# Optimization experiments

Measured on AMD Instinct MI355X. Metric: run time of the kernel, lower is better.

The kernel has to match this reference:

```python
import jax, jax.numpy as jnp
import numpy as np

N_HOPS = 2
TOPK = 10
LAMBDA = 0.5  # lambda_coeff
N_ENT = 8192
N_USR = 16384
CHANNEL = 64
N_EDGE = 1000000
NNZ = 500000
N_REL = 9


def _l2norm(x, eps=1e-12):
    # F.normalize: x / max(||x||, eps) per row
    n = jnp.linalg.norm(x, axis=-1, keepdims=True)
    return x / jnp.maximum(n, eps)


def build_adj(context, topk):
    n = context.shape[0]
    cn = context / jnp.linalg.norm(context, axis=-1, keepdims=True)
    sim = cn @ cn.T                                   # [N,N]
    knn_val, knn_ind = jax.lax.top_k(sim, topk)        # [N,topk]
    rows = jnp.repeat(jnp.arange(n), topk)
    cols = knn_ind.reshape(-1)
    vals = knn_val.reshape(-1)
    rowsum = knn_val.sum(axis=1)                       # sparse row sums
    dinv = rowsum ** -0.5
    vals = dinv[rows] * vals * dinv[cols]              # D^-1/2 A D^-1/2
    return jnp.zeros((n, n), context.dtype).at[rows, cols].add(vals)


def aggregate(entity_emb, user_emb, head, tail, i_rows, i_cols, inter_vals, weight, edge_type):
    n_ent = entity_emb.shape[0]
    n_usr = user_emb.shape[0]
    rel = weight[edge_type - 1]                        # [E,C]
    h_emb = entity_emb[head]
    t_emb = entity_emb[tail]
    neigh = t_emb * rel                                # [E,C]
    # attention weight: (||h*r|| * ||t*r||)^2 per edge
    att = (jnp.linalg.norm(h_emb * rel, axis=1) * jnp.linalg.norm(t_emb * rel, axis=1)) ** 2
    # scatter_softmax over head segments
    m = jax.ops.segment_max(att, head, num_segments=n_ent)
    e = jnp.exp(att - m[head])
    denom = jax.ops.segment_sum(e, head, num_segments=n_ent)
    w = (e / denom[head])[:, None]                     # [E,1], broadcast == expand
    entity_agg = jax.ops.segment_sum(w * neigh, head, num_segments=n_ent)
    # sparse mm: interact_mat @ entity_emb
    user_agg = jax.ops.segment_sum(inter_vals[:, None] * entity_emb[i_cols], i_rows, num_segments=n_usr)
    score = jax.nn.softmax(user_emb @ weight.T, axis=-1)
    user_agg = user_agg + (score @ weight) * user_agg
    return entity_agg, user_agg


def setup_inputs() -> dict:
    key = jax.random.key(0)
    k = jax.random.split(key, 7)
    user_emb = jax.random.normal(k[0], (N_USR, CHANNEL), jnp.float32) * 0.1
    entity_emb = jax.random.normal(k[1], (N_ENT, CHANNEL), jnp.float32) * 0.1
    edge_index = jax.random.randint(k[2], (2, N_EDGE), 0, N_ENT)
    edge_type = jax.random.randint(k[3], (N_EDGE,), 0, N_REL - 1) + 1  # in [1, n_relations-1]
    inter_rows = jax.random.randint(k[4], (NNZ,), 0, N_USR)
    inter_cols = jax.random.randint(k[5], (NNZ,), 0, N_ENT)
    inter_indices = jnp.stack([inter_rows, inter_cols], axis=0)
    inter_vals = jax.random.uniform(k[6], (NNZ,), jnp.float32)
    # xavier-uniform-like relation weight
    bound = float(np.sqrt(6.0 / (N_REL - 1 + CHANNEL)))
    weight = jax.random.uniform(jax.random.fold_in(key, 7), (N_REL - 1, CHANNEL), jnp.float32, -bound, bound)
    return {"user_emb": user_emb, "entity_emb": entity_emb, "edge_index": edge_index,
            "edge_type": edge_type, "inter_indices": inter_indices,
            "inter_vals": inter_vals, "weight": weight}


def reference(user_emb, entity_emb, edge_index, edge_type, inter_indices, inter_vals, weight):
    head, tail = edge_index[0], edge_index[1]
    i_rows, i_cols = inter_indices[0], inter_indices[1]
    origin_item_adj = build_adj(entity_emb, TOPK)
    entity_res_emb = entity_emb
    user_res_emb = user_emb
    for _ in range(N_HOPS):
        entity_emb, user_emb = aggregate(entity_emb, user_emb, head, tail,
                                         i_rows, i_cols, inter_vals, weight, edge_type)
        entity_emb = _l2norm(entity_emb)
        user_emb = _l2norm(user_emb)
        entity_res_emb = entity_res_emb + entity_emb
        user_res_emb = user_res_emb + user_emb
    item_adj = (1.0 - LAMBDA) * build_adj(entity_res_emb, TOPK) + LAMBDA * origin_item_adj
    return entity_res_emb, user_res_emb, item_adj
```

## Files before the change

### kernel.cpp

```cpp
#include <hip/hip_runtime.h>
#include <hip/hip_bf16.h>

#define N_ENT   8192
#define N_USR   16384
#define CH      64
#define N_EDGEC 1000000
#define NNZC    500000
#define TOPKC   10
#define NRELM1  8
#define KSPLIT  384
#define BKS     96
#define LDSP    104
#define LDSTP   133
#define NTILE   64
#define NTRI    2080

typedef __bf16 bf16x8 __attribute__((ext_vector_type(8)));
typedef float  f32x4  __attribute__((ext_vector_type(4)));

static __device__ __forceinline__ float waveReduceSum(float v){
#pragma unroll
  for(int o=1;o<64;o<<=1) v += __shfl_xor(v,o,64);
  return v;
}
static __device__ __forceinline__ float waveReduceMax(float v){
#pragma unroll
  for(int o=1;o<64;o<<=1) v = fmaxf(v, __shfl_xor(v,o,64));
  return v;
}
static __device__ __forceinline__ unsigned long long u64max(unsigned long long a, unsigned long long b){
  return a>b? a: b;
}
static __device__ __forceinline__ unsigned mapf(float v){
  unsigned u = __float_as_uint(v);
  return (u & 0x80000000u) ? ~u : (u | 0x80000000u);
}
static __device__ __forceinline__ float unmapf(unsigned mk){
  unsigned uo = (mk & 0x80000000u) ? (mk ^ 0x80000000u) : ~mk;
  return __uint_as_float(uo);
}
static __device__ __forceinline__ ushort f2bf(float x){
  unsigned u = __float_as_uint(x);
  return (ushort)((u + 0x7FFFu + ((u>>16)&1u)) >> 16);
}
static __device__ __forceinline__ float bf2f(ushort h){
  return __uint_as_float((unsigned)h<<16);
}

__global__ void k_hist(const int* __restrict__ keys, int n, int* __restrict__ hist){
  int i = blockIdx.x*blockDim.x + threadIdx.x;
  int stride = gridDim.x*blockDim.x;
  for(; i<n; i+=stride) atomicAdd(&hist[keys[i]], 1);
}

__global__ __launch_bounds__(1024) void k_scan(const int* __restrict__ hist,
                                               int* __restrict__ start,
                                               int* __restrict__ cursor, int n){
  __shared__ int part[1024];
  int t = threadIdx.x;
  int chunk = n/1024;
  int base = t*chunk;
  int s = 0;
  for(int i=0;i<chunk;i++) s += hist[base+i];
  part[t] = s; __syncthreads();
  for(int off=1; off<1024; off<<=1){
    int v = (t>=off) ? part[t-off] : 0;
    __syncthreads();
    part[t] += v;
    __syncthreads();
  }
  int run = (t==0) ? 0 : part[t-1];
  for(int i=0;i<chunk;i++){
    start[base+i] = run; cursor[base+i] = run;
    run += hist[base+i];
  }
  if(t==1023) start[n] = run;
}

__global__ void k_scatter_sortE(const int* __restrict__ head,
                                const int* __restrict__ tail,
                                const int* __restrict__ etype, int n,
                                int* __restrict__ cursor, int* __restrict__ trS){
  int i = blockIdx.x*blockDim.x + threadIdx.x;
  int stride = gridDim.x*blockDim.x;
  for(; i<n; i+=stride){
    int pos = atomicAdd(&cursor[head[i]], 1);
    trS[pos] = (tail[i] & 8191) | ((etype[i]-1)<<13);
  }
}

__global__ void k_scatter_sortU(const int* __restrict__ irows,
                                const int* __restrict__ icols,
                                const float* __restrict__ ivals, int n,
                                int* __restrict__ cursor,
                                int* __restrict__ icolsS, float* __restrict__ ivalsS){
  int i = blockIdx.x*blockDim.x + threadIdx.x;
  int stride = gridDim.x*blockDim.x;
  for(; i<n; i+=stride){
    int pos = atomicAdd(&cursor[irows[i]], 1);
    icolsS[pos] = icols[i];
    ivalsS[pos] = ivals[i];
  }
}

__global__ __launch_bounds__(256) void k_split(const float* __restrict__ in,
                                               ushort* __restrict__ outA,
                                               ushort* __restrict__ outB){
  int wave = threadIdx.x>>6, lane = threadIdx.x&63;
  int r = blockIdx.x*4 + wave;
  float v = in[(size_t)r*CH+lane];
  float ss = waveReduceSum(v*v);
  float x = v / sqrtf(ss);
  ushort h = f2bf(x);
  float r1 = x - bf2f(h);
  ushort m = f2bf(r1);
  float r2 = r1 - bf2f(m);
  ushort l = f2bf(r2);
  ushort* oA = outA + (size_t)r*KSPLIT;
  ushort* oB = outB + (size_t)r*KSPLIT;
  oA[lane]     =h; oA[64+lane] =h; oA[128+lane]=m;
  oA[192+lane] =l; oA[256+lane]=h; oA[320+lane]=m;
  oB[lane]     =h; oB[64+lane] =m; oB[128+lane]=h;
  oB[192+lane] =h; oB[256+lane]=l; oB[320+lane]=m;
}

__global__ __launch_bounds__(256) void k_gemm_bf16(const ushort* __restrict__ A,
                                                   const ushort* __restrict__ B,
                                                   float* __restrict__ C,
                                                   float* __restrict__ rowmax){
  __shared__ __align__(16) ushort As[128*LDSP];
  __shared__ __align__(16) ushort Bs[128*LDSP];
  const int tid = threadIdx.x, lane = tid&63, wid = tid>>6;

  int bid = blockIdx.x;
  int by = (int)((129.0f - sqrtf(16641.0f - 8.0f*(float)bid)) * 0.5f);
  while(((by+1)*64 - ((by+1)*by)/2) <= bid) by++;
  while((by*64 - (by*(by-1))/2) > bid) by--;
  int bx = by + (bid - (by*64 - (by*(by-1))/2));

  const int bi = by*128, bj = bx*128;
  const int wr = (wid>>1)*64, wc = (wid&1)*64;
  const int r16 = lane&15, kg = lane>>4;

  f32x4 acc[4][4] = {};

  const uint4* gA = (const uint4*)A + (size_t)bi*(KSPLIT/8);
  const uint4* gB = (const uint4*)B + (size_t)bj*(KSPLIT/8);
  const int row2 = tid>>1, half = tid&1;

  for(int s=0; s<KSPLIT/BKS; ++s){
    __syncthreads();
#pragma unroll
    for(int jj=0;jj<6;jj++){
      *(uint4*)&As[row2*LDSP + half*48 + jj*8] = gA[row2*(KSPLIT/8) + s*12 + half*6 + jj];
      *(uint4*)&Bs[row2*LDSP + half*48 + jj*8] = gB[row2*(KSPLIT/8) + s*12 + half*6 + jj];
    }
    __syncthreads();
#pragma unroll
    for(int kk=0;kk<3;kk++){
      bf16x8 a[4], b[4];
#pragma unroll
      for(int m=0;m<4;m++)
        a[m] = *(const bf16x8*)&As[(wr+m*16+r16)*LDSP + kk*32 + kg*8];
#pragma unroll
      for(int n=0;n<4;n++)
        b[n] = *(const bf16x8*)&Bs[(wc+n*16+r16)*LDSP + kk*32 + kg*8];
#pragma unroll
      for(int m=0;m<4;m++)
#pragma unroll
        for(int n=0;n<4;n++)
          acc[m][n] = __builtin_amdgcn_mfma_f32_16x16x32_bf16(a[m], b[n], acc[m][n], 0,0,0);
    }
  }

#pragma unroll
  for(int m=0;m<4;m++){
#pragma unroll
    for(int n=0;n<4;n++){
      size_t base = (size_t)(bi + wr + m*16 + kg*4)*N_ENT + (bj + wc + n*16 + r16);
      C[base]          = acc[m][n][0];
      C[base+N_ENT]    = acc[m][n][1];
      C[base+2*N_ENT]  = acc[m][n][2];
      C[base+3*N_ENT]  = acc[m][n][3];
    }
  }

  float tmax[4][4];
#pragma unroll
  for(int m=0;m<4;m++){
#pragma unroll
    for(int rg=0;rg<4;rg++){
      float v = acc[m][0][rg];
      v = fmaxf(v, acc[m][1][rg]);
      v = fmaxf(v, acc[m][2][rg]);
      v = fmaxf(v, acc[m][3][rg]);
#pragma unroll
      for(int o=1;o<16;o<<=1) v = fmaxf(v, __shfl_xor(v, o, 64));
      tmax[m][rg] = v;
    }
  }
  float cm[4];
#pragma unroll
  for(int n=0;n<4;n++){
    float v = acc[0][n][0];
#pragma unroll
    for(int m=0;m<4;m++)
#pragma unroll
      for(int rg=0;rg<4;rg++) v = fmaxf(v, acc[m][n][rg]);
    v = fmaxf(v, __shfl_xor(v, 16, 64));
    v = fmaxf(v, __shfl_xor(v, 32, 64));
    cm[n] = v;
  }

  __syncthreads();
  float* rm  = (float*)Bs;
  float* cmb = ((float*)Bs) + 128;
  if(((wid&1)==0) && r16==0){
#pragma unroll
    for(int m=0;m<4;m++)
#pragma unroll
      for(int rg=0;rg<4;rg++)
        rm[wr + m*16 + kg*4 + rg] = tmax[m][rg];
  }
  if(wid<2 && kg==0){
#pragma unroll
    for(int n=0;n<4;n++) cmb[wc + n*16 + r16] = cm[n];
  }
  __syncthreads();
  if(((wid&1)==1) && r16==0){
#pragma unroll
    for(int m=0;m<4;m++)
#pragma unroll
      for(int rg=0;rg<4;rg++){
        int rrow = wr + m*16 + kg*4 + rg;
        rowmax[(size_t)(bi+rrow)*NTILE + bx] = fmaxf(tmax[m][rg], rm[rrow]);
      }
  }
  if(by != bx && wid>=2 && kg==0){
#pragma unroll
    for(int n=0;n<4;n++){
      int ccol = wc + n*16 + r16;
      rowmax[(size_t)(bj+ccol)*NTILE + by] = fmaxf(cm[n], cmb[ccol]);
    }
  }

  if(by != bx){
    float* ldsT = (float*)As;
    for(int q=0;q<4;q++){
      __syncthreads();
#pragma unroll
      for(int n=0;n<4;n++){
        if(((wc>>5) + (n>>1)) == q){
          int cl = ((n&1)*16) + r16;
#pragma unroll
          for(int m=0;m<4;m++)
#pragma unroll
            for(int rg=0;rg<4;rg++)
              ldsT[cl*LDSTP + wr + m*16 + kg*4 + rg] = acc[m][n][rg];
        }
      }
      __syncthreads();
      int cr = tid>>3;
      int g  = tid&7;
      float* crow = C + (size_t)(bj + q*32 + cr)*N_ENT + bi;
#pragma unroll
      for(int f=0; f<4; ++f){
        int cidx = (g + f*8)*4;
        float4 v = *(float4*)&ldsT[cr*LDSTP + cidx];
        *(float4*)&crow[cidx] = v;
      }
    }
  }
}

#define CANDCAP 256
__global__ __launch_bounds__(64) void k_topk(const float* __restrict__ S,
                                             const float* __restrict__ rowmax,
                                             int* __restrict__ knn_idx,
                                             float* __restrict__ knn_val,
                                             float* __restrict__ rowsum){
  const int row = blockIdx.x;
  const int lane = threadIdx.x;
  const float4* s4 = (const float4*)(S + (size_t)row*N_ENT);

  __shared__ unsigned long long cand[CANDCAP];
  __shared__ int tlist[NTILE];
  __shared__ int cnt, tcnt;
  if(lane==0){ cnt=0; tcnt=0; }
  __syncthreads();

  float tm = rowmax[(size_t)row*NTILE + lane];
  unsigned long long work = ((unsigned long long)mapf(tm)<<32) | (unsigned)lane;
  unsigned long long w = 0;
  for(int sel=0; sel<TOPKC; ++sel){
    w = work;
#pragma unroll
    for(int o=1;o<64;o<<=1) w = u64max(w, __shfl_xor(w,o,64));
    if(work == w) work = 0ull;
  }
  float tauf = unmapf((unsigned)(w>>32));

  if(tm >= tauf){ int p = atomicAdd(&tcnt,1); tlist[p] = lane; }
  __syncthreads();
  int nt = tcnt;

  for(int i = (lane>>5); i < nt; i += 2){
    int t  = tlist[i];
    int fo = lane&31;
    float4 v = s4[t*32 + fo];
    int c0 = t*128 + fo*4;
    float vv[4] = {v.x,v.y,v.z,v.w};
#pragma unroll
    for(int j=0;j<4;j++){
      if(vv[j] >= tauf){
        int pos = atomicAdd(&cnt,1);
        if(pos < CANDCAP)
          cand[pos] = ((unsigned long long)mapf(vv[j])<<32)
                    | (unsigned long long)(0xFFFFFFFFu - (unsigned)(c0+j));
      }
    }
  }
  __syncthreads();
  int n = cnt;

  if(n <= CANDCAP){
    unsigned long long c0 = (lane      < n) ? cand[lane]       : 0ull;
    unsigned long long c1 = (lane+64   < n) ? cand[lane+64]    : 0ull;
    unsigned long long c2 = (lane+128  < n) ? cand[lane+128]   : 0ull;
    unsigned long long c3 = (lane+192  < n) ? cand[lane+192]   : 0ull;
    float rs = 0.f;
    for(int sel=0; sel<TOPKC; ++sel){
      unsigned long long m = u64max(u64max(c0,c1), u64max(c2,c3));
#pragma unroll
      for(int o=1;o<64;o<<=1) m = u64max(m, __shfl_xor(m,o,64));
      if(c0==m) c0=0ull; else if(c1==m) c1=0ull;
      else if(c2==m) c2=0ull; else if(c3==m) c3=0ull;
      if(lane==0){
        float v = unmapf((unsigned)(m>>32));
        int col = (int)(0xFFFFFFFFu - (unsigned)(m & 0xFFFFFFFFu));
        knn_idx[row*TOPKC+sel] = col;
        knn_val[row*TOPKC+sel] = v;
        rs += v;
      }
    }
    if(lane==0) rowsum[row] = rs;
  } else {
    unsigned long long loc[TOPKC];
#pragma unroll
    for(int i=0;i<TOPKC;i++) loc[i]=0ull;
    for(int it=0; it<N_ENT/256; ++it){
      int vi = it*64+lane;
      float4 v = s4[vi];
      int c0i = vi*4;
      float vv[4] = {v.x,v.y,v.z,v.w};
#pragma unroll
      for(int j=0;j<4;j++){
        unsigned u = mapf(vv[j]);
        unsigned long long key = ((unsigned long long)u<<32)
                               | (unsigned long long)(0xFFFFFFFFu - (unsigned)(c0i+j));
        if(key > loc[TOPKC-1]){
          unsigned long long t = key;
#pragma unroll
          for(int z=0; z<TOPKC; ++z){
            if(t > loc[z]){ unsigned long long tmp=loc[z]; loc[z]=t; t=tmp; }
          }
        }
      }
    }
    float rs = 0.f;
    for(int sel=0; sel<TOPKC; ++sel){
      unsigned long long m = loc[0];
#pragma unroll
      for(int o=1;o<64;o<<=1) m = u64max(m, __shfl_xor(m,o,64));
      if(loc[0] == m){
#pragma unroll
        for(int z=0;z<TOPKC-1;++z) loc[z]=loc[z+1];
        loc[TOPKC-1]=0ull;
      }
      if(lane==0){
        float v = unmapf((unsigned)(m>>32));
        int col = (int)(0xFFFFFFFFu - (unsigned)(m & 0xFFFFFFFFu));
        knn_idx[row*TOPKC+sel] = col;
        knn_val[row*TOPKC+sel] = v;
        rs += v;
      }
    }
    if(lane==0) rowsum[row] = rs;
  }
}

__global__ __launch_bounds__(256) void k_q(const float* __restrict__ ent,
                                           const float* __restrict__ W,
                                           float* __restrict__ q){
  int wave=threadIdx.x>>6, lane=threadIdx.x&63;
  int r = blockIdx.x*4+wave;
  if(r>=N_ENT) return;
  float x = ent[(size_t)r*CH+lane];
#pragma unroll
  for(int rel=0; rel<NRELM1; rel++){
    float tt = x*W[rel*CH+lane];
    float s = waveReduceSum(tt*tt);
    if(lane==0) q[r*NRELM1+rel]=s;
  }
}

__global__ __launch_bounds__(256) void k_edge_agg(
    const int* __restrict__ trS, const int* __restrict__ startE,
    const float* __restrict__ ent, const float* __restrict__ W,
    const float* __restrict__ q, float* __restrict__ wbuf,
    float* __restrict__ agg){
  int wave=threadIdx.x>>6, lane=threadIdx.x&63;
  int h = blockIdx.x*4+wave;
  if(h>=N_ENT) return;
  int s = startE[h], e2 = startE[h+1];

  float qh[NRELM1];
#pragma unroll
  for(int r=0;r<NRELM1;r++) qh[r] = q[h*NRELM1+r];

  float mx = 0.f;
  for(int p=s+lane; p<e2; p+=64){
    int tr = trS[p];
    int tl = tr & 8191, r = tr>>13;
    float att = qh[r]*q[tl*NRELM1+r];
    wbuf[p] = att;
    mx = fmaxf(mx, att);
  }
  mx = waveReduceMax(mx);

  float dn = 0.f;
  for(int p=s+lane; p<e2; p+=64){
    float e = expf(wbuf[p]-mx);
    wbuf[p] = e;
    dn += e;
  }
  dn = waveReduceSum(dn);
  float inv = (dn>0.f) ? 1.f/dn : 0.f;

  float wr[NRELM1];
#pragma unroll
  for(int r=0;r<NRELM1;r++) wr[r] = W[r*CH+lane];
  float acc = 0.f;
  for(int p=s; p<e2; p++){
    int tr = trS[p];
    int tl = tr & 8191, r = tr>>13;
    float wgt = wbuf[p]*inv;
    acc = fmaf(wgt*wr[r], ent[(size_t)tl*CH+lane], acc);
  }
  agg[(size_t)h*CH+lane] = acc;
}

__global__ __launch_bounds__(256) void k_user(
    const int* __restrict__ icolsS, const float* __restrict__ ivalsS,
    const int* __restrict__ startU,
    const float* __restrict__ ent, const float* __restrict__ W,
    float* __restrict__ usr, float* __restrict__ usr_res){
  int wave=threadIdx.x>>6, lane=threadIdx.x&63;
  int u = blockIdx.x*4+wave;
  if(u>=N_USR) return;
  float ue = usr[(size_t)u*CH+lane];
  float l[NRELM1];
#pragma unroll
  for(int r=0;r<NRELM1;r++) l[r] = waveReduceSum(ue*W[r*CH+lane]);
  float lm = l[0];
#pragma unroll
  for(int r=1;r<NRELM1;r++) lm = fmaxf(lm,l[r]);
  float se=0.f;
#pragma unroll
  for(int r=0;r<NRELM1;r++){ l[r]=expf(l[r]-lm); se+=l[r]; }
  float inv = 1.f/se;
  float g = 0.f;
#pragma unroll
  for(int r=0;r<NRELM1;r++) g = fmaf(l[r]*inv, W[r*CH+lane], g);
  float acc=0.f;
  int s=startU[u], e2=startU[u+1];
  for(int p=s;p<e2;p++){
    acc = fmaf(ivalsS[p], ent[(size_t)icolsS[p]*CH+lane], acc);
  }
  float res = acc*(1.f+g);
  float nrm = sqrtf(waveReduceSum(res*res));
  float outv = res / fmaxf(nrm, 1e-12f);
  usr_res[(size_t)u*CH+lane] += outv;
  usr[(size_t)u*CH+lane] = outv;
}

__global__ __launch_bounds__(256) void k_entfin(const float* __restrict__ agg,
                                                float* __restrict__ cur,
                                                float* __restrict__ res){
  int wave=threadIdx.x>>6, lane=threadIdx.x&63;
  int r = blockIdx.x*4+wave;
  if(r>=N_ENT) return;
  float v = agg[(size_t)r*CH+lane];
  float nrm = sqrtf(waveReduceSum(v*v));
  float outv = v / fmaxf(nrm, 1e-12f);
  cur[(size_t)r*CH+lane]=outv;
  res[(size_t)r*CH+lane]+=outv;
}

__global__ __launch_bounds__(256) void k_write_adj(
    const int* __restrict__ ki0, const float* __restrict__ kv0,
    const float* __restrict__ rs0,
    const int* __restrict__ ki1, const float* __restrict__ kv1,
    const float* __restrict__ rs1,
    float* __restrict__ adj){
  const int row = blockIdx.x;
  const int t = threadIdx.x;
  __shared__ int   cols[2*TOPKC];
  __shared__ float vals[2*TOPKC];

  if(t < TOPKC){
    int c = ki1[row*TOPKC+t];
    cols[t] = c;
    vals[t] = 0.5f * kv1[row*TOPKC+t] / (sqrtf(rs1[row]) * sqrtf(rs1[c]));
  } else if(t < 2*TOPKC){
    int i = t - TOPKC;
    int c = ki0[row*TOPKC+i];
    cols[t] = c;
    vals[t] = 0.5f * kv0[row*TOPKC+i] / (sqrtf(rs0[row]) * sqrtf(rs0[c]));
  }
  __syncthreads();
  if(t==0){
    for(int i=TOPKC;i<2*TOPKC;i++){
      int c = cols[i];
      for(int j=0;j<TOPKC;j++){
        if(cols[j]==c){ vals[j]+=vals[i]; cols[i]=-1; break; }
      }
    }
  }
  __syncthreads();

  float4* adj4 = (float4*)(adj + (size_t)row*N_ENT);
  float4 z = {0.f,0.f,0.f,0.f};
#pragma unroll
  for(int k=0;k<8;k++) adj4[k*256 + t] = z;
  __syncthreads();
  if(t < 2*TOPKC){
    int c = cols[t];
    if(c >= 0) adj[(size_t)row*N_ENT + c] = vals[t];
  }
}

extern "C" void kernel_launch(void* const* d_in, const int* in_sizes, int n_in,
                              void* d_out, int out_size, void* d_ws, size_t ws_size,
                              hipStream_t stream){
  const float* user_emb   = (const float*)d_in[0];
  const float* entity_emb = (const float*)d_in[1];
  const int*   edge_index = (const int*)d_in[2];
  const int*   edge_type  = (const int*)d_in[3];
  const int*   inter_idx  = (const int*)d_in[4];
  const float* inter_vals = (const float*)d_in[5];
  const float* W          = (const float*)d_in[6];

  const int* head  = edge_index;
  const int* tail  = edge_index + N_EDGEC;
  const int* irows = inter_idx;
  const int* icols = inter_idx + NNZC;

  float* out     = (float*)d_out;
  float* ent_res = out;
  float* usr_res = out + (size_t)N_ENT*CH;
  float* adj     = out + (size_t)N_ENT*CH + (size_t)N_USR*CH;

  char* wp = (char*)d_ws;
  auto alloc = [&](size_t bytes)->void*{
    void* p = (void*)wp; wp += (bytes+255)/256*256; return p;
  };
  ushort* abufA  = (ushort*)alloc((size_t)N_ENT*KSPLIT*2);
  ushort* abufB  = (ushort*)alloc((size_t)N_ENT*KSPLIT*2);
  float* rowmax  = (float*)alloc((size_t)N_ENT*NTILE*4);
  float* cur_ent = (float*)alloc((size_t)N_ENT*CH*4);
  float* cur_usr = (float*)alloc((size_t)N_USR*CH*4);
  float* agg     = (float*)alloc((size_t)N_ENT*CH*4);
  float* q       = (float*)alloc((size_t)N_ENT*NRELM1*4);
  int*   histE   = (int*)alloc((size_t)N_ENT*4);
  int*   startE  = (int*)alloc((size_t)(N_ENT+1)*4);
  int*   cursorE = (int*)alloc((size_t)N_ENT*4);
  int*   trS     = (int*)alloc((size_t)N_EDGEC*4);
  int*   histU   = (int*)alloc((size_t)N_USR*4);
  int*   startU  = (int*)alloc((size_t)(N_USR+1)*4);
  int*   cursorU = (int*)alloc((size_t)N_USR*4);
  int*   icolsS  = (int*)alloc((size_t)NNZC*4);
  float* ivalsS  = (float*)alloc((size_t)NNZC*4);
  int*   knn_idx0= (int*)alloc((size_t)N_ENT*TOPKC*4);
  float* knn_val0= (float*)alloc((size_t)N_ENT*TOPKC*4);
  float* rowsum0 = (float*)alloc((size_t)N_ENT*4);
  int*   knn_idx1= (int*)alloc((size_t)N_ENT*TOPKC*4);
  float* knn_val1= (float*)alloc((size_t)N_ENT*TOPKC*4);
  float* rowsum1 = (float*)alloc((size_t)N_ENT*4);

  float* wbuf = adj;

  hipMemsetAsync(histE, 0, (size_t)N_ENT*4, stream);
  hipMemsetAsync(histU, 0, (size_t)N_USR*4, stream);
  hipMemcpyAsync(ent_res, entity_emb, (size_t)N_ENT*CH*4, hipMemcpyDeviceToDevice, stream);
  hipMemcpyAsync(usr_res, user_emb,   (size_t)N_USR*CH*4, hipMemcpyDeviceToDevice, stream);
  hipMemcpyAsync(cur_ent, entity_emb, (size_t)N_ENT*CH*4, hipMemcpyDeviceToDevice, stream);
  hipMemcpyAsync(cur_usr, user_emb,   (size_t)N_USR*CH*4, hipMemcpyDeviceToDevice, stream);

  k_hist<<<1024,256,0,stream>>>(head, N_EDGEC, histE);
  k_hist<<<512,256,0,stream>>>(irows, NNZC, histU);
  k_scan<<<1,1024,0,stream>>>(histE, startE, cursorE, N_ENT);
  k_scan<<<1,1024,0,stream>>>(histU, startU, cursorU, N_USR);
  k_scatter_sortE<<<1024,256,0,stream>>>(head, tail, edge_type, N_EDGEC, cursorE, trS);
  k_scatter_sortU<<<512,256,0,stream>>>(irows, icols, inter_vals, NNZC, cursorU, icolsS, ivalsS);

  k_split<<<N_ENT/4,256,0,stream>>>(entity_emb, abufA, abufB);
  k_gemm_bf16<<<NTRI,256,0,stream>>>(abufA, abufB, adj, rowmax);
  k_topk<<<N_ENT,64,0,stream>>>(adj, rowmax, knn_idx0, knn_val0, rowsum0);

  for(int hop=0; hop<2; ++hop){
    k_q<<<N_ENT/4,256,0,stream>>>(cur_ent, W, q);
    k_edge_agg<<<N_ENT/4,256,0,stream>>>(trS, startE, cur_ent, W, q, wbuf, agg);
    k_user<<<N_USR/4,256,0,stream>>>(icolsS, ivalsS, startU, cur_ent, W, cur_usr, usr_res);
    k_entfin<<<N_ENT/4,256,0,stream>>>(agg, cur_ent, ent_res);
  }

  k_split<<<N_ENT/4,256,0,stream>>>(ent_res, abufA, abufB);
  k_gemm_bf16<<<NTRI,256,0,stream>>>(abufA, abufB, adj, rowmax);
  k_topk<<<N_ENT,64,0,stream>>>(adj, rowmax, knn_idx1, knn_val1, rowsum1);

  k_write_adj<<<N_ENT,256,0,stream>>>(knn_idx0, knn_val0, rowsum0,
                                      knn_idx1, knn_val1, rowsum1, adj);
}
```

Measured before the change: 826.5 us.

## Fuse softmax into single edge pass, fold q computation into entfin, merge init copies

The edge aggregation now computes exp(att) and the running denominator in one pass over each head's edges, dropping the max-subtraction pass and the wbuf round trip through global memory. This is numerically safe only while att stays small, which holds for L2-normalized embeddings times small relation weights. The per-hop k_q kernel is folded into k_entfin for the second hop, and four device-to-device memcpys are replaced by one vectorized init kernel. The aim is fewer launches and less memory traffic, at the cost of no overflow protection in the exp.

```diff
diff --git a/kernel.cpp b/kernel.cpp
--- a/kernel.cpp
+++ b/kernel.cpp
@@ -23,11 +23,6 @@
   for(int o=1;o<64;o<<=1) v += __shfl_xor(v,o,64);
   return v;
 }
-static __device__ __forceinline__ float waveReduceMax(float v){
-#pragma unroll
-  for(int o=1;o<64;o<<=1) v = fmaxf(v, __shfl_xor(v,o,64));
-  return v;
-}
 static __device__ __forceinline__ unsigned long long u64max(unsigned long long a, unsigned long long b){
   return a>b? a: b;
 }
@@ -45,6 +40,23 @@
 }
 static __device__ __forceinline__ float bf2f(ushort h){
   return __uint_as_float((unsigned)h<<16);
+}
+
+__global__ __launch_bounds__(256) void k_init(const float* __restrict__ ue,
+                                              const float* __restrict__ ee,
+                                              float* __restrict__ usr_res,
+                                              float* __restrict__ cur_usr,
+                                              float* __restrict__ ent_res,
+                                              float* __restrict__ cur_ent){
+  int i = blockIdx.x*256 + threadIdx.x;
+  float4 v = ((const float4*)ue)[i];
+  ((float4*)usr_res)[i] = v;
+  ((float4*)cur_usr)[i] = v;
+  if(i < N_ENT*(CH/4)){
+    float4 w = ((const float4*)ee)[i];
+    ((float4*)ent_res)[i] = w;
+    ((float4*)cur_ent)[i] = w;
+  }
 }
 
 __global__ void k_hist(const int* __restrict__ keys, int n, int* __restrict__ hist){
@@ -407,8 +419,7 @@
 __global__ __launch_bounds__(256) void k_edge_agg(
     const int* __restrict__ trS, const int* __restrict__ startE,
     const float* __restrict__ ent, const float* __restrict__ W,
-    const float* __restrict__ q, float* __restrict__ wbuf,
-    float* __restrict__ agg){
+    const float* __restrict__ q, float* __restrict__ agg){
   int wave=threadIdx.x>>6, lane=threadIdx.x&63;
   int h = blockIdx.x*4+wave;
   if(h>=N_ENT) return;
@@ -417,37 +428,21 @@
   float qh[NRELM1];
 #pragma unroll
   for(int r=0;r<NRELM1;r++) qh[r] = q[h*NRELM1+r];
-
-  float mx = 0.f;
-  for(int p=s+lane; p<e2; p+=64){
-    int tr = trS[p];
-    int tl = tr & 8191, r = tr>>13;
-    float att = qh[r]*q[tl*NRELM1+r];
-    wbuf[p] = att;
-    mx = fmaxf(mx, att);
-  }
-  mx = waveReduceMax(mx);
+  float wr[NRELM1];
+#pragma unroll
+  for(int r=0;r<NRELM1;r++) wr[r] = W[r*CH+lane];
 
   float dn = 0.f;
-  for(int p=s+lane; p<e2; p+=64){
-    float e = expf(wbuf[p]-mx);
-    wbuf[p] = e;
-    dn += e;
-  }
-  dn = waveReduceSum(dn);
-  float inv = (dn>0.f) ? 1.f/dn : 0.f;
-
-  float wr[NRELM1];
-#pragma unroll
-  for(int r=0;r<NRELM1;r++) wr[r] = W[r*CH+lane];
   float acc = 0.f;
   for(int p=s; p<e2; p++){
     int tr = trS[p];
     int tl = tr & 8191, r = tr>>13;
-    float wgt = wbuf[p]*inv;
-    acc = fmaf(wgt*wr[r], ent[(size_t)tl*CH+lane], acc);
-  }
-  agg[(size_t)h*CH+lane] = acc;
+    float e = expf(qh[r]*q[tl*NRELM1+r]);
+    dn += e;
+    acc = fmaf(e*wr[r], ent[(size_t)tl*CH+lane], acc);
+  }
+  float inv = (dn>0.f) ? 1.f/dn : 0.f;
+  agg[(size_t)h*CH+lane] = acc*inv;
 }
 
 __global__ __launch_bounds__(256) void k_user(
@@ -486,7 +481,9 @@
 
 __global__ __launch_bounds__(256) void k_entfin(const float* __restrict__ agg,
                                                 float* __restrict__ cur,
-                                                float* __restrict__ res){
+                                                float* __restrict__ res,
+                                                const float* __restrict__ W,
+                                                float* __restrict__ q, int makeq){
   int wave=threadIdx.x>>6, lane=threadIdx.x&63;
   int r = blockIdx.x*4+wave;
   if(r>=N_ENT) return;
@@ -495,6 +492,14 @@
   float outv = v / fmaxf(nrm, 1e-12f);
   cur[(size_t)r*CH+lane]=outv;
   res[(size_t)r*CH+lane]+=outv;
+  if(makeq){
+#pragma unroll
+    for(int rel=0; rel<NRELM1; rel++){
+      float tt = outv*W[rel*CH+lane];
+      float s = waveReduceSum(tt*tt);
+      if(lane==0) q[r*NRELM1+rel]=s;
+    }
+  }
 }
 
 __global__ __launch_bounds__(256) void k_write_adj(
@@ -588,14 +593,10 @@
   float* knn_val1= (float*)alloc((size_t)N_ENT*TOPKC*4);
   float* rowsum1 = (float*)alloc((size_t)N_ENT*4);
 
-  float* wbuf = adj;
-
   hipMemsetAsync(histE, 0, (size_t)N_ENT*4, stream);
   hipMemsetAsync(histU, 0, (size_t)N_USR*4, stream);
-  hipMemcpyAsync(ent_res, entity_emb, (size_t)N_ENT*CH*4, hipMemcpyDeviceToDevice, stream);
-  hipMemcpyAsync(usr_res, user_emb,   (size_t)N_USR*CH*4, hipMemcpyDeviceToDevice, stream);
-  hipMemcpyAsync(cur_ent, entity_emb, (size_t)N_ENT*CH*4, hipMemcpyDeviceToDevice, stream);
-  hipMemcpyAsync(cur_usr, user_emb,   (size_t)N_USR*CH*4, hipMemcpyDeviceToDevice, stream);
+  k_init<<<N_USR*(CH/4)/256,256,0,stream>>>(user_emb, entity_emb,
+                                            usr_res, cur_usr, ent_res, cur_ent);
 
   k_hist<<<1024,256,0,stream>>>(head, N_EDGEC, histE);
   k_hist<<<512,256,0,stream>>>(irows, NNZC, histU);
@@ -608,11 +609,11 @@
   k_gemm_bf16<<<NTRI,256,0,stream>>>(abufA, abufB, adj, rowmax);
   k_topk<<<N_ENT,64,0,stream>>>(adj, rowmax, knn_idx0, knn_val0, rowsum0);
 
+  k_q<<<N_ENT/4,256,0,stream>>>(cur_ent, W, q);
   for(int hop=0; hop<2; ++hop){
-    k_q<<<N_ENT/4,256,0,stream>>>(cur_ent, W, q);
-    k_edge_agg<<<N_ENT/4,256,0,stream>>>(trS, startE, cur_ent, W, q, wbuf, agg);
+    k_edge_agg<<<N_ENT/4,256,0,stream>>>(trS, startE, cur_ent, W, q, agg);
     k_user<<<N_USR/4,256,0,stream>>>(icolsS, ivalsS, startU, cur_ent, W, cur_usr, usr_res);
-    k_entfin<<<N_ENT/4,256,0,stream>>>(agg, cur_ent, ent_res);
+    k_entfin<<<N_ENT/4,256,0,stream>>>(agg, cur_ent, ent_res, W, q, hop==0);
   }
 
   k_split<<<N_ENT/4,256,0,stream>>>(ent_res, abufA, abufB);
```

New measurement: 887.3 us. +7.3%, slower.
